# Optimization experiments

Measured on AMD Instinct MI355X. Metric: run time of the kernel, lower is better.

The kernel has to match this reference:

```python
import jax, jax.numpy as jnp
import numpy as np

B, KB, SEQ, HID = 8, 16, 512, 768  # batch, two_times_batch, max_length, hidden
NEG_INF = float('-inf')


def _l2_normalize(x, eps=1e-12):
    # torch F.normalize: x / max(||x||_2, eps)
    n = jnp.sqrt(jnp.sum(x * x, axis=-1, keepdims=True))
    return x / jnp.maximum(n, eps)


def setup_inputs() -> dict:
    key = jax.random.key(0)
    k1, k2, k3, k4 = jax.random.split(key, 4)
    return {
        'query_embs': jax.random.normal(k1, (B, SEQ, HID), dtype=jnp.float32),
        'key_embs': jax.random.normal(k2, (KB, SEQ, HID), dtype=jnp.float32),
        'alpha_raw': jnp.float32(0.1),  # learnable scalar, cfg.model.alpha init
        'q_mask': jax.random.randint(k3, (B, SEQ), 0, 2, dtype=jnp.int32),
        'k_mask': jax.random.randint(k4, (KB, SEQ), 0, 2, dtype=jnp.int32),
    }


def reference(query_embs, key_embs, alpha_raw, q_mask, k_mask):
    # cfg: distance_weightning='exp', use_softmax=True, gumbel_temp=None
    qn = _l2_normalize(query_embs)          # [B, S, H]
    kn = _l2_normalize(key_embs)            # [KB, T, H]

    # cosine similarity: [B, KB, S, T]
    sim = jnp.einsum('ish,jth->ijst', qn, kn)

    # exp distance weighting, alpha = leaky_relu(alpha_raw)
    alpha = jax.nn.leaky_relu(alpha_raw)
    pos = jnp.arange(SEQ, dtype=jnp.float32)
    distance = jnp.abs(pos[:, None] - pos[None, :])        # [S, T]
    sim = sim * jnp.exp(-alpha * distance)

    valid = (q_mask[:, None, :, None] != 0) & (k_mask[None, :, None, :] != 0)
    logits = jnp.where(valid, sim, NEG_INF)

    p = jax.nn.softmax(logits, axis=-1)                    # [B, KB, S, T]
    p = jnp.nan_to_num(p, nan=0.0)

    # aggregate normalized keys under attention, dot with queries
    aggregated = jnp.einsum('ijst,jth->ijsh', p, kn)       # [B, KB, S, H]
    scores = jnp.einsum('ish,ijsh->ijs', qn, aggregated)   # [B, KB, S]
    scores = scores * q_mask[:, None, :].astype(scores.dtype)
    return scores.sum(axis=-1)                             # [B, KB]
```

## Files before the change

### kernel.cpp

```cpp
#include <hip/hip_runtime.h>

#define B_   8
#define KB_  16
#define SEQ_ 512
#define HID_ 768

typedef __attribute__((ext_vector_type(4))) _Float16 half4;
typedef __attribute__((ext_vector_type(8))) _Float16 half8;
typedef __attribute__((ext_vector_type(4))) float    floatx4;

__global__ __launch_bounds__(256)
void prep_kernel(const float* __restrict__ Q, const float* __restrict__ K,
                 _Float16* __restrict__ Qh, _Float16* __restrict__ Kh)
{
    int row  = blockIdx.x * 4 + (threadIdx.x >> 6);
    int lane = threadIdx.x & 63;
    const float* src;
    _Float16*    dst;
    if (row < B_ * SEQ_) { src = Q + (size_t)row * HID_;              dst = Qh + (size_t)row * HID_; }
    else                 { src = K + (size_t)(row - B_*SEQ_) * HID_;  dst = Kh + (size_t)(row - B_*SEQ_) * HID_; }

    float4 v[3];
    float s = 0.f;
#pragma unroll
    for (int it = 0; it < 3; ++it) {
        v[it] = *(const float4*)(src + lane * 4 + it * 256);
        s += v[it].x * v[it].x + v[it].y * v[it].y + v[it].z * v[it].z + v[it].w * v[it].w;
    }
#pragma unroll
    for (int m = 1; m < 64; m <<= 1) s += __shfl_xor(s, m, 64);
    float sc = 1.0f / fmaxf(sqrtf(s), 1e-12f);
#pragma unroll
    for (int it = 0; it < 3; ++it) {
        half4 h = { (_Float16)(v[it].x * sc), (_Float16)(v[it].y * sc),
                    (_Float16)(v[it].z * sc), (_Float16)(v[it].w * sc) };
        *(half4*)(dst + lane * 4 + it * 256) = h;
    }
}

#define BM  128
#define BN  128
#define BK  32
#define LDH 40

__global__ __launch_bounds__(256, 3)
void li_part(const _Float16* __restrict__ Qh, const _Float16* __restrict__ Kh,
             const float* __restrict__ alpha_p, const int* __restrict__ kmask,
             float* __restrict__ Pbuf)
{
    const int st = blockIdx.x >> 2;
    const int tb = blockIdx.x & 3;
    const int j  = blockIdx.y;
    const int i  = blockIdx.z;

    const _Float16* Qi = Qh + ((size_t)i * SEQ_ + st * BM) * HID_;
    const _Float16* Kj = Kh + ((size_t)j * SEQ_ + tb * BN) * HID_;
    const int* km = kmask + j * SEQ_ + tb * BN;

    __shared__ _Float16 Qs[BM * LDH];
    __shared__ _Float16 Ks[BN * LDH];
    __shared__ float pm[2][BM], pl[2][BM], pn[2][BM];

    const int tid  = threadIdx.x;
    const int lane = tid & 63;
    const int wave = tid >> 6;
    const int quad = lane >> 4;
    const int l16  = lane & 15;
    const int wr   = wave >> 1;
    const int wc   = wave & 1;

    const float araw  = *alpha_p;
    const float alpha = araw >= 0.f ? araw : 0.01f * araw;

    floatx4 acc[4][4];
#pragma unroll
    for (int rt = 0; rt < 4; ++rt)
#pragma unroll
        for (int ct = 0; ct < 4; ++ct)
            acc[rt][ct] = (floatx4){0.f, 0.f, 0.f, 0.f};

    const int sr0 = tid >> 2;
    const int sk0 = (tid & 3) * 8;

    for (int k0 = 0; k0 < HID_; k0 += BK) {
        half8 q0  = *(const half8*)(Qi + (size_t)sr0 * HID_ + k0 + sk0);
        half8 q1  = *(const half8*)(Qi + (size_t)(sr0 + 64) * HID_ + k0 + sk0);
        half8 kv0 = *(const half8*)(Kj + (size_t)sr0 * HID_ + k0 + sk0);
        half8 kv1 = *(const half8*)(Kj + (size_t)(sr0 + 64) * HID_ + k0 + sk0);
        __syncthreads();
        *(half8*)(Qs + sr0 * LDH + sk0)        = q0;
        *(half8*)(Qs + (sr0 + 64) * LDH + sk0) = q1;
        *(half8*)(Ks + sr0 * LDH + sk0)        = kv0;
        *(half8*)(Ks + (sr0 + 64) * LDH + sk0) = kv1;
        __syncthreads();

        half8 af[4], bf[4];
#pragma unroll
        for (int rt = 0; rt < 4; ++rt)
            af[rt] = *(const half8*)(Qs + (wr * 64 + rt * 16 + l16) * LDH + quad * 8);
#pragma unroll
        for (int ct = 0; ct < 4; ++ct)
            bf[ct] = *(const half8*)(Ks + (wc * 64 + ct * 16 + l16) * LDH + quad * 8);
#pragma unroll
        for (int rt = 0; rt < 4; ++rt)
#pragma unroll
            for (int ct = 0; ct < 4; ++ct)
                acc[rt][ct] = __builtin_amdgcn_mfma_f32_16x16x32_f16(af[rt], bf[ct], acc[rt][ct], 0, 0, 0);
    }

    int kmv[4]; float tgf[4];
#pragma unroll
    for (int ct = 0; ct < 4; ++ct) {
        int t_loc = wc * 64 + ct * 16 + l16;
        kmv[ct] = km[t_loc];
        tgf[ct] = (float)(tb * BN + t_loc);
    }
#pragma unroll
    for (int rt = 0; rt < 4; ++rt) {
#pragma unroll
        for (int r = 0; r < 4; ++r) {
            float sgf = (float)(st * BM + wr * 64 + rt * 16 + quad * 4 + r);
            float cv[4], w[4];
            float tmax = -INFINITY;
#pragma unroll
            for (int ct = 0; ct < 4; ++ct) {
                cv[ct] = acc[rt][ct][r];
                float d = fabsf(sgf - tgf[ct]);
                w[ct] = kmv[ct] ? cv[ct] * __expf(-alpha * d) : -INFINITY;
                tmax = fmaxf(tmax, w[ct]);
            }
#pragma unroll
            for (int msk = 1; msk < 16; msk <<= 1)
                tmax = fmaxf(tmax, __shfl_xor(tmax, msk, 64));
            float ps = 0.f, ns = 0.f;
            if (tmax != -INFINITY) {
#pragma unroll
                for (int ct = 0; ct < 4; ++ct) {
                    float e = __expf(w[ct] - tmax);
                    ps += e;
                    ns += e * cv[ct];
                }
#pragma unroll
                for (int msk = 1; msk < 16; msk <<= 1) {
                    ps += __shfl_xor(ps, msk, 64);
                    ns += __shfl_xor(ns, msk, 64);
                }
            }
            if (l16 == 0) {
                int rloc = wr * 64 + rt * 16 + quad * 4 + r;
                pm[wc][rloc] = tmax;
                pl[wc][rloc] = ps;
                pn[wc][rloc] = ns;
            }
        }
    }
    __syncthreads();

    if (tid < BM) {
        float m0 = pm[0][tid], m1 = pm[1][tid];
        float M = fmaxf(m0, m1);
        float l = 0.f, n = 0.f;
        if (M != -INFINITY) {
            float e0 = __expf(m0 - M), e1 = __expf(m1 - M);
            l = pl[0][tid] * e0 + pl[1][tid] * e1;
            n = pn[0][tid] * e0 + pn[1][tid] * e1;
        }
        size_t base = (((size_t)(i * KB_ + j) * SEQ_) + st * BM + tid) * 12 + tb * 3;
        Pbuf[base]     = M;
        Pbuf[base + 1] = l;
        Pbuf[base + 2] = n;
    }
}

__global__ __launch_bounds__(256)
void li_reduce(const float* __restrict__ Pbuf, const int* __restrict__ qmask,
               float* __restrict__ out)
{
    const int ij = blockIdx.x;
    const int i  = ij >> 4;
    const int tid = threadIdx.x;
    __shared__ float red[4];

    float sum = 0.f;
#pragma unroll
    for (int rep = 0; rep < 2; ++rep) {
        int s = tid + rep * 256;
        const float4* p = (const float4*)(Pbuf + ((size_t)ij * SEQ_ + s) * 12);
        float4 a = p[0], b = p[1], c = p[2];
        float M = fmaxf(fmaxf(a.x, a.w), fmaxf(b.z, c.y));
        float sc = 0.f;
        if (M != -INFINITY) {
            float e0 = __expf(a.x - M), e1 = __expf(a.w - M);
            float e2 = __expf(b.z - M), e3 = __expf(c.y - M);
            float l = a.y * e0 + b.x * e1 + b.w * e2 + c.z * e3;
            float n = a.z * e0 + b.y * e1 + c.x * e2 + c.w * e3;
            sc = (l > 0.f) ? n / l : 0.f;
        }
        if (qmask[i * SEQ_ + s] == 0) sc = 0.f;
        sum += sc;
    }
#pragma unroll
    for (int m = 1; m < 64; m <<= 1) sum += __shfl_xor(sum, m, 64);
    if ((tid & 63) == 0) red[tid >> 6] = sum;
    __syncthreads();
    if (tid == 0) out[ij] = red[0] + red[1] + red[2] + red[3];
}

extern "C" void kernel_launch(void* const* d_in, const int* in_sizes, int n_in,
                              void* d_out, int out_size, void* d_ws, size_t ws_size,
                              hipStream_t stream)
{
    const float* Q       = (const float*)d_in[0];
    const float* K       = (const float*)d_in[1];
    const float* alpha_p = (const float*)d_in[2];
    const int*   qmask   = (const int*)d_in[3];
    const int*   kmask   = (const int*)d_in[4];
    float*       out     = (float*)d_out;

    char* ws = (char*)d_ws;
    _Float16* Qh   = (_Float16*)ws;
    _Float16* Kh   = (_Float16*)(ws + (size_t)B_ * SEQ_ * HID_ * 2);
    float*    Pbuf = (float*)   (ws + (size_t)(B_ + KB_) * SEQ_ * HID_ * 2);

    prep_kernel<<<(B_ + KB_) * SEQ_ / 4, 256, 0, stream>>>(Q, K, Qh, Kh);

    dim3 grid(16, KB_, B_);
    li_part<<<grid, 256, 0, stream>>>(Qh, Kh, alpha_p, kmask, Pbuf);

    li_reduce<<<B_ * KB_, 256, 0, stream>>>(Pbuf, qmask, out);
}
```

Before: 167.2 us.

## Pre-swizzle normalized Q/K into MFMA fragment layout and load directly from global

The prep kernel now writes the fp16 normalized rows in a tiled layout where each 16-row by 32-column block is stored contiguously in MFMA operand order. The GEMM kernel drops its LDS staging and both barriers per k-step, and each wave loads its A/B fragments straight from global memory as coalesced 16-byte loads. This removes shared-memory traffic and synchronisation, but data is no longer shared between waves through LDS, so more global/L2 reads are issued and there is no explicit prefetching across k-steps.

```diff
diff --git a/kernel.cpp b/kernel.cpp
--- a/kernel.cpp
+++ b/kernel.cpp
@@ -5,46 +5,70 @@
 #define SEQ_ 512
 #define HID_ 768
 
+#define NKB  (HID_ / 32)
+#define QRB  (B_  * SEQ_ / 16)
+#define KRB  (KB_ * SEQ_ / 16)
+
 typedef __attribute__((ext_vector_type(4))) _Float16 half4;
 typedef __attribute__((ext_vector_type(8))) _Float16 half8;
 typedef __attribute__((ext_vector_type(4))) float    floatx4;
 
+#define LP 776
+
 __global__ __launch_bounds__(256)
-void prep_kernel(const float* __restrict__ Q, const float* __restrict__ K,
-                 _Float16* __restrict__ Qh, _Float16* __restrict__ Kh)
-{
-    int row  = blockIdx.x * 4 + (threadIdx.x >> 6);
-    int lane = threadIdx.x & 63;
+void prep_tile(const float* __restrict__ Q, const float* __restrict__ K,
+               _Float16* __restrict__ Qt, _Float16* __restrict__ Kt)
+{
+    const int rb = blockIdx.x;
     const float* src;
     _Float16*    dst;
-    if (row < B_ * SEQ_) { src = Q + (size_t)row * HID_;              dst = Qh + (size_t)row * HID_; }
-    else                 { src = K + (size_t)(row - B_*SEQ_) * HID_;  dst = Kh + (size_t)(row - B_*SEQ_) * HID_; }
-
-    float4 v[3];
-    float s = 0.f;
-#pragma unroll
-    for (int it = 0; it < 3; ++it) {
-        v[it] = *(const float4*)(src + lane * 4 + it * 256);
-        s += v[it].x * v[it].x + v[it].y * v[it].y + v[it].z * v[it].z + v[it].w * v[it].w;
-    }
-#pragma unroll
-    for (int m = 1; m < 64; m <<= 1) s += __shfl_xor(s, m, 64);
-    float sc = 1.0f / fmaxf(sqrtf(s), 1e-12f);
-#pragma unroll
-    for (int it = 0; it < 3; ++it) {
-        half4 h = { (_Float16)(v[it].x * sc), (_Float16)(v[it].y * sc),
-                    (_Float16)(v[it].z * sc), (_Float16)(v[it].w * sc) };
-        *(half4*)(dst + lane * 4 + it * 256) = h;
+    if (rb < QRB) { src = Q + (size_t)rb * 16 * HID_;          dst = Qt + (size_t)rb * NKB * 512; }
+    else          { src = K + (size_t)(rb - QRB) * 16 * HID_;  dst = Kt + (size_t)(rb - QRB) * NKB * 512; }
+
+    __shared__ _Float16 Ls[16 * LP];
+    const int wave = threadIdx.x >> 6;
+    const int lane = threadIdx.x & 63;
+
+#pragma unroll
+    for (int rr = 0; rr < 4; ++rr) {
+        int row = wave * 4 + rr;
+        const float* s = src + (size_t)row * HID_;
+        float4 v[3];
+        float ss = 0.f;
+#pragma unroll
+        for (int it = 0; it < 3; ++it) {
+            v[it] = *(const float4*)(s + lane * 4 + it * 256);
+            ss += v[it].x * v[it].x + v[it].y * v[it].y + v[it].z * v[it].z + v[it].w * v[it].w;
+        }
+#pragma unroll
+        for (int m = 1; m < 64; m <<= 1) ss += __shfl_xor(ss, m, 64);
+        float sc = 1.0f / fmaxf(sqrtf(ss), 1e-12f);
+#pragma unroll
+        for (int it = 0; it < 3; ++it) {
+            half4 h = { (_Float16)(v[it].x * sc), (_Float16)(v[it].y * sc),
+                        (_Float16)(v[it].z * sc), (_Float16)(v[it].w * sc) };
+            *(half4*)(Ls + row * LP + lane * 4 + it * 256) = h;
+        }
+    }
+    __syncthreads();
+
+#pragma unroll
+    for (int rep = 0; rep < 6; ++rep) {
+        int slot = rep * 256 + threadIdx.x;
+        int kb   = slot >> 6;
+        int ln   = slot & 63;
+        int row  = ln & 15;
+        int ko   = kb * 32 + (ln >> 4) * 8;
+        half8 h = *(const half8*)(Ls + row * LP + ko);
+        *(half8*)(dst + (size_t)kb * 512 + (size_t)ln * 8) = h;
     }
 }
 
 #define BM  128
 #define BN  128
-#define BK  32
-#define LDH 40
 
 __global__ __launch_bounds__(256, 3)
-void li_part(const _Float16* __restrict__ Qh, const _Float16* __restrict__ Kh,
+void li_part(const _Float16* __restrict__ Qt, const _Float16* __restrict__ Kt,
              const float* __restrict__ alpha_p, const int* __restrict__ kmask,
              float* __restrict__ Pbuf)
 {
@@ -52,14 +76,6 @@
     const int tb = blockIdx.x & 3;
     const int j  = blockIdx.y;
     const int i  = blockIdx.z;
-
-    const _Float16* Qi = Qh + ((size_t)i * SEQ_ + st * BM) * HID_;
-    const _Float16* Kj = Kh + ((size_t)j * SEQ_ + tb * BN) * HID_;
-    const int* km = kmask + j * SEQ_ + tb * BN;
-
-    __shared__ _Float16 Qs[BM * LDH];
-    __shared__ _Float16 Ks[BN * LDH];
-    __shared__ float pm[2][BM], pl[2][BM], pn[2][BM];
 
     const int tid  = threadIdx.x;
     const int lane = tid & 63;
@@ -69,9 +85,14 @@
     const int wr   = wave >> 1;
     const int wc   = wave & 1;
 
+    __shared__ float pm[2][BM], pl[2][BM], pn[2][BM];
+
     const float araw  = *alpha_p;
     const float alpha = araw >= 0.f ? araw : 0.01f * araw;
 
+    const _Float16* Abase = Qt + ((size_t)(i * 32 + st * 8 + wr * 4) * NKB) * 512 + (size_t)lane * 8;
+    const _Float16* Bbase = Kt + ((size_t)(j * 32 + tb * 8 + wc * 4) * NKB) * 512 + (size_t)lane * 8;
+
     floatx4 acc[4][4];
 #pragma unroll
     for (int rt = 0; rt < 4; ++rt)
@@ -79,28 +100,14 @@
         for (int ct = 0; ct < 4; ++ct)
             acc[rt][ct] = (floatx4){0.f, 0.f, 0.f, 0.f};
 
-    const int sr0 = tid >> 2;
-    const int sk0 = (tid & 3) * 8;
-
-    for (int k0 = 0; k0 < HID_; k0 += BK) {
-        half8 q0  = *(const half8*)(Qi + (size_t)sr0 * HID_ + k0 + sk0);
-        half8 q1  = *(const half8*)(Qi + (size_t)(sr0 + 64) * HID_ + k0 + sk0);
-        half8 kv0 = *(const half8*)(Kj + (size_t)sr0 * HID_ + k0 + sk0);
-        half8 kv1 = *(const half8*)(Kj + (size_t)(sr0 + 64) * HID_ + k0 + sk0);
-        __syncthreads();
-        *(half8*)(Qs + sr0 * LDH + sk0)        = q0;
-        *(half8*)(Qs + (sr0 + 64) * LDH + sk0) = q1;
-        *(half8*)(Ks + sr0 * LDH + sk0)        = kv0;
-        *(half8*)(Ks + (sr0 + 64) * LDH + sk0) = kv1;
-        __syncthreads();
-
+    for (int kb = 0; kb < NKB; ++kb) {
         half8 af[4], bf[4];
 #pragma unroll
         for (int rt = 0; rt < 4; ++rt)
-            af[rt] = *(const half8*)(Qs + (wr * 64 + rt * 16 + l16) * LDH + quad * 8);
+            af[rt] = *(const half8*)(Abase + ((size_t)rt * NKB + kb) * 512);
 #pragma unroll
         for (int ct = 0; ct < 4; ++ct)
-            bf[ct] = *(const half8*)(Ks + (wc * 64 + ct * 16 + l16) * LDH + quad * 8);
+            bf[ct] = *(const half8*)(Bbase + ((size_t)ct * NKB + kb) * 512);
 #pragma unroll
         for (int rt = 0; rt < 4; ++rt)
 #pragma unroll
@@ -108,6 +115,7 @@
                 acc[rt][ct] = __builtin_amdgcn_mfma_f32_16x16x32_f16(af[rt], bf[ct], acc[rt][ct], 0, 0, 0);
     }
 
+    const int* km = kmask + j * SEQ_ + tb * BN;
     int kmv[4]; float tgf[4];
 #pragma unroll
     for (int ct = 0; ct < 4; ++ct) {
@@ -218,14 +226,14 @@
     float*       out     = (float*)d_out;
 
     char* ws = (char*)d_ws;
-    _Float16* Qh   = (_Float16*)ws;
-    _Float16* Kh   = (_Float16*)(ws + (size_t)B_ * SEQ_ * HID_ * 2);
+    _Float16* Qt   = (_Float16*)ws;
+    _Float16* Kt   = (_Float16*)(ws + (size_t)B_ * SEQ_ * HID_ * 2);
     float*    Pbuf = (float*)   (ws + (size_t)(B_ + KB_) * SEQ_ * HID_ * 2);
 
-    prep_kernel<<<(B_ + KB_) * SEQ_ / 4, 256, 0, stream>>>(Q, K, Qh, Kh);
+    prep_tile<<<QRB + KRB, 256, 0, stream>>>(Q, K, Qt, Kt);
 
     dim3 grid(16, KB_, B_);
-    li_part<<<grid, 256, 0, stream>>>(Qh, Kh, alpha_p, kmask, Pbuf);
+    li_part<<<grid, 256, 0, stream>>>(Qt, Kt, alpha_p, kmask, Pbuf);
 
     li_reduce<<<B_ * KB_, 256, 0, stream>>>(Pbuf, qmask, out);
 }
```

After: 187.8 us. 12.3% more time.
